# Optimization experiments

Hardware: AMD Instinct MI355X
Metric: run time of the kernel (lower is better)

Reference implementation:

```python
import jax, jax.numpy as jnp
import numpy as np

FREQ_DIM = 64
BLOCK_DIM = 64
N = 256          # lattice sites
CH = 6           # channel_num -> block diagonals at offsets -1, 0, +1
S = 2 * 16 + CH - 2   # seq_num = 36
BS = 4           # block_size (kron of two 2x2 matrices)
HID = 128
EPS = 1e-5
B = 32

_e = np.eye(2)
_sx = np.array([[0., 1.], [1., 0.]])
_siy = np.array([[0., 1.], [-1., 0.]])
_sz = np.array([[1., 0.], [0., -1.]])
_p = [_e, _sx, _siy, _sz]
KRONS = jnp.asarray(np.stack([np.kron(_p[a], _p[b]) for a in range(4) for b in range(4)]).astype(np.float32))  # (16,4,4)
Z1 = KRONS[12]  # kron(sigma_z, I) used for interaction blocks ('z1')


def _bn(h, g, b):
    # BatchNorm1d in training mode: biased batch statistics over axis 0
    mu = h.mean(axis=0)
    v = h.var(axis=0)
    return g * (h - mu) / jnp.sqrt(v + EPS) + b


def _mlp(x, Win, bin_, Wmid, bmid, Wout, bout, gamma, beta):
    # depth-4 MLP: Lin+ReLU, then (BN,Lin,ReLU) x2, then BN,Lin,ReLU
    h = jax.nn.relu(x @ Win + bin_)
    for i in range(Wmid.shape[0]):
        h = jax.nn.relu(_bn(h, gamma[i], beta[i]) @ Wmid[i] + bmid[i])
    return jax.nn.relu(_bn(h, gamma[-1], beta[-1]) @ Wout + bout)


def _lstm(xs, h0, c0, Wih, Whh, bih, bhh):
    # xs: (B, T, S); torch gate order i, f, g, o
    def step(carry, x_t):
        h, c = carry
        gates = x_t @ Wih.T + h @ Whh.T + (bih + bhh)
        i, f, g, o = jnp.split(gates, 4, axis=-1)
        c = jax.nn.sigmoid(f) * c + jax.nn.sigmoid(i) * jnp.tanh(g)
        h = jax.nn.sigmoid(o) * jnp.tanh(c)
        return (h, c), h
    _, hs = jax.lax.scan(step, (h0, c0), jnp.swapaxes(xs, 0, 1))
    return jnp.swapaxes(hs, 0, 1)


def setup_inputs() -> dict:
    key = jax.random.key(0)
    ks = iter(jax.random.split(key, 48))
    def w(shape, s=0.05):
        return jax.random.normal(next(ks), shape, dtype=jnp.float32) * s
    d = {
        'x': w((B, FREQ_DIM + BLOCK_DIM), 1.0),
        'fd_Win': w((FREQ_DIM, HID)), 'fd_bin': w((HID,)),
        'fd_Wmid': w((2, HID, HID)), 'fd_bmid': w((2, HID)),
        'fd_Wout': w((HID, S)), 'fd_bout': w((S,)),
        'fd_gamma': jnp.ones((3, HID), jnp.float32), 'fd_beta': jnp.zeros((3, HID), jnp.float32),
        'bd_Win': w((BLOCK_DIM, HID)), 'bd_bin': w((HID,)),
        'bd_Wmid': w((2, HID, HID)), 'bd_bmid': w((2, HID)),
        'bd_Wout': w((HID, S)), 'bd_bout': w((S,)),
        'bd_gamma': jnp.ones((3, HID), jnp.float32), 'bd_beta': jnp.zeros((3, HID), jnp.float32),
        'sc_Win': w((S, 1, HID)), 'sc_bin': w((S, HID)),
        'sc_Wmid': w((S, 2, HID, HID)), 'sc_bmid': w((S, 2, HID)),
        'sc_Wout': w((S, HID, N)), 'sc_bout': w((S, N)),
        'sc_gamma': jnp.ones((S, 3, HID), jnp.float32), 'sc_beta': jnp.zeros((S, 3, HID), jnp.float32),
        'lstm_Wih': w((4 * S, S)), 'lstm_Whh': w((4 * S, S)),
        'lstm_bih': w((4 * S,)), 'lstm_bhh': w((4 * S,)),
        'mix_W': w((S, 2 * S)), 'mix_b': w((S,)),
    }
    return d


def reference(x, fd_Win, fd_bin, fd_Wmid, fd_bmid, fd_Wout, fd_bout, fd_gamma, fd_beta,
              bd_Win, bd_bin, bd_Wmid, bd_bmid, bd_Wout, bd_bout, bd_gamma, bd_beta,
              sc_Win, sc_bin, sc_Wmid, sc_bmid, sc_Wout, sc_bout, sc_gamma, sc_beta,
              lstm_Wih, lstm_Whh, lstm_bih, lstm_bhh, mix_W, mix_b):
    Bsz = x.shape[0]
    block = _mlp(x[:, FREQ_DIM:], bd_Win, bd_bin, bd_Wmid, bd_bmid, bd_Wout, bd_bout, bd_gamma, bd_beta)  # (B,S)
    freq = _mlp(x[:, :FREQ_DIM], fd_Win, fd_bin, fd_Wmid, fd_bmid, fd_Wout, fd_bout, fd_gamma, fd_beta)   # (B,S)
    # S independent scalar->N MLPs, batched with vmap over the stacked params
    sc = jax.vmap(_mlp)(freq.T[:, :, None], sc_Win, sc_bin, sc_Wmid, sc_bmid,
                        sc_Wout, sc_bout, sc_gamma, sc_beta)  # (S,B,N)
    freq_seq = jnp.cos(sc).transpose(1, 2, 0)   # (B,N,S)
    seq = _lstm(freq_seq, block, jnp.zeros_like(block), lstm_Wih, lstm_Whh, lstm_bih, lstm_bhh)  # (B,N,S)
    block_seq = jnp.concatenate([jnp.broadcast_to(block[:, :, None], (Bsz, S, N)),
                                 jnp.swapaxes(seq, 1, 2)], axis=1)  # (B,2S,N)
    # 1x1 Conv2d == channel mixing matmul
    mixed = jnp.einsum('bcn,oc->bon', block_seq, mix_W) + mix_b[None, :, None]  # (B,S,N)
    inter = mixed[:, :CH - 2]                          # (B,CH-2,N)
    onsite = mixed[:, CH - 2:].reshape(Bsz, 2, 16, N)  # (B,2,16,N)
    H_int = jnp.einsum('bcn,ij->bcnij', inter, Z1)         # (B,CH-2,N,4,4)
    H_os = jnp.einsum('bgkn,kij->bgnij', onsite, KRONS)    # (B,2,N,4,4) summed over 16 pairs
    half = (CH - 2) // 2
    strips = jnp.concatenate([H_int[:, :half], H_os, H_int[:, half:]], axis=1)  # (B,CH,N,4,4)
    strips = strips.reshape(Bsz, CH // 2, 2, N, BS, BS)
    # banded block assembly: strip i lives on block-diagonal offset i - (CH//2)//2
    grid = jnp.zeros((Bsz, 2, N, N, BS, BS), dtype=x.dtype)
    for i in range(CH // 2):
        o = i - (CH // 2) // 2
        rows = jnp.arange(N - abs(o)) + max(0, -o)
        cols = rows + o
        grid = grid.at[:, :, rows, cols].set(strips[:, i][:, :, rows])
    matrix = grid.transpose(0, 1, 2, 4, 3, 5).reshape(Bsz, 2, N * BS, N * BS)
    return matrix
```

## Files before the change

### kernel.cpp

```cpp
#include <hip/hip_runtime.h>
#include <math.h>

#define EPSF 1e-5f
typedef __attribute__((ext_vector_type(2))) float f32x2;
typedef __attribute__((ext_vector_type(4))) float f32x4;

__device__ __forceinline__ float pauliv(int p, int r, int c) {
    switch (p) {
        case 0: return (r == c) ? 1.f : 0.f;
        case 1: return (r != c) ? 1.f : 0.f;
        case 2: return (r == 0 && c == 1) ? 1.f : ((r == 1 && c == 0) ? -1.f : 0.f);
        default: return (r == c) ? ((r == 0) ? 1.f : -1.f) : 0.f;
    }
}

__device__ void mlp64_body(const float* __restrict__ xin,
                           const float* __restrict__ Win,
                           const float* __restrict__ bin_,
                           const float* __restrict__ Wmid,
                           const float* __restrict__ bmid,
                           const float* __restrict__ Wout,
                           const float* __restrict__ bout,
                           const float* __restrict__ gamma,
                           const float* __restrict__ beta,
                           float* __restrict__ out)
{
    __shared__ float sX[2048];
    __shared__ float sA[4096];
    __shared__ float sB[4096];
    __shared__ float sMu[128], sRs[128];
    int tid = threadIdx.x;

    for (int idx = tid; idx < 2048; idx += 512) {
        int b = idx >> 6, c = idx & 63;
        sX[idx] = xin[b * 128 + c];
    }
    __syncthreads();

    for (int idx = tid; idx < 4096; idx += 512) {
        int b = idx >> 7, j = idx & 127;
        float acc = bin_[j];
        for (int c = 0; c < 64; ++c) acc = fmaf(sX[b * 64 + c], Win[c * 128 + j], acc);
        sA[idx] = fmaxf(acc, 0.f);
    }
    __syncthreads();

    float* cur = sA;
    float* nxt = sB;
    for (int l = 0; l < 3; ++l) {
        if (tid < 128) {
            float s = 0.f, s2 = 0.f;
            for (int b = 0; b < 32; ++b) {
                float v = cur[b * 128 + tid];
                s += v; s2 += v * v;
            }
            float mu = s * (1.f / 32.f);
            float var = s2 * (1.f / 32.f) - mu * mu;
            sMu[tid] = mu;
            sRs[tid] = rsqrtf(var + EPSF);
        }
        __syncthreads();
        for (int idx = tid; idx < 4096; idx += 512) {
            int j = idx & 127;
            cur[idx] = gamma[l * 128 + j] * (cur[idx] - sMu[j]) * sRs[j] + beta[l * 128 + j];
        }
        __syncthreads();
        if (l < 2) {
            for (int idx = tid; idx < 4096; idx += 512) {
                int b = idx >> 7, j = idx & 127;
                float acc = bmid[l * 128 + j];
                for (int c = 0; c < 128; ++c)
                    acc = fmaf(cur[b * 128 + c], Wmid[(l * 128 + c) * 128 + j], acc);
                nxt[idx] = fmaxf(acc, 0.f);
            }
            __syncthreads();
            float* t = cur; cur = nxt; nxt = t;
        } else {
            for (int idx = tid; idx < 1152; idx += 512) {
                int b = idx / 36, j = idx - b * 36;
                float acc = bout[j];
                for (int c = 0; c < 128; ++c)
                    acc = fmaf(cur[b * 128 + c], Wout[c * 36 + j], acc);
                out[idx] = fmaxf(acc, 0.f);
            }
        }
    }
}

__global__ __launch_bounds__(512) void k_mlp2(
    const float* __restrict__ x,
    const float* fdWin, const float* fdbin, const float* fdWmid, const float* fdbmid,
    const float* fdWout, const float* fdbout, const float* fdg, const float* fdbt,
    const float* bdWin, const float* bdbin, const float* bdWmid, const float* bdbmid,
    const float* bdWout, const float* bdbout, const float* bdg, const float* bdbt,
    float* freq, float* blk)
{
    if (blockIdx.x == 0)
        mlp64_body(x + 64, bdWin, bdbin, bdWmid, bdbmid, bdWout, bdbout, bdg, bdbt, blk);
    else
        mlp64_body(x, fdWin, fdbin, fdWmid, fdbmid, fdWout, fdbout, fdg, fdbt, freq);
}

__global__ __launch_bounds__(512) void k_sc1(
    const float* __restrict__ freq,
    const float* __restrict__ Win,
    const float* __restrict__ bin_,
    const float* __restrict__ Wmid,
    const float* __restrict__ bmid,
    const float* __restrict__ gamma,
    const float* __restrict__ beta,
    float* __restrict__ actW)
{
    int s = blockIdx.x, tid = threadIdx.x;
    __shared__ float sA[4096];
    __shared__ float sB[4096];
    __shared__ float sMu[128], sRs[128];
    const float* Wm = Wmid + (size_t)s * 2 * 128 * 128;
    const float* gm = gamma + s * 3 * 128;
    const float* bt = beta + s * 3 * 128;

    for (int idx = tid; idx < 4096; idx += 512) {
        int b = idx >> 7, j = idx & 127;
        float acc = fmaf(freq[b * 36 + s], Win[s * 128 + j], bin_[s * 128 + j]);
        sA[idx] = fmaxf(acc, 0.f);
    }
    __syncthreads();

    float* cur = sA;
    float* nxt = sB;
    for (int l = 0; l < 3; ++l) {
        if (tid < 128) {
            float sm = 0.f, s2 = 0.f;
            for (int b = 0; b < 32; ++b) {
                float v = cur[b * 128 + tid];
                sm += v; s2 += v * v;
            }
            float mu = sm * (1.f / 32.f);
            float var = s2 * (1.f / 32.f) - mu * mu;
            sMu[tid] = mu;
            sRs[tid] = rsqrtf(var + EPSF);
        }
        __syncthreads();
        for (int idx = tid; idx < 4096; idx += 512) {
            int j = idx & 127;
            cur[idx] = gm[l * 128 + j] * (cur[idx] - sMu[j]) * sRs[j] + bt[l * 128 + j];
        }
        __syncthreads();
        if (l < 2) {
            int jj = tid & 127, bb = tid >> 7;
            float acc[8];
            #pragma unroll
            for (int k = 0; k < 8; ++k) acc[k] = bmid[(s * 2 + l) * 128 + jj];
            for (int c = 0; c < 128; ++c) {
                float w = Wm[(l * 128 + c) * 128 + jj];
                #pragma unroll
                for (int k = 0; k < 8; ++k)
                    acc[k] = fmaf(cur[(bb + 4 * k) * 128 + c], w, acc[k]);
            }
            __syncthreads();
            #pragma unroll
            for (int k = 0; k < 8; ++k) nxt[(bb + 4 * k) * 128 + jj] = fmaxf(acc[k], 0.f);
            __syncthreads();
            float* t = cur; cur = nxt; nxt = t;
        } else {
            for (int idx = tid; idx < 4096; idx += 512)
                actW[(size_t)s * 4096 + idx] = cur[idx];
        }
    }
}

__global__ __launch_bounds__(512) void k_sc2(
    const float* __restrict__ actW,
    const float* __restrict__ Wout,
    const float* __restrict__ bout,
    float* __restrict__ fseq2)
{
    int bidx = blockIdx.x;
    int s = bidx >> 2, q = bidx & 3;
    int tid = threadIdx.x;
    __shared__ float sAct[4096];
    for (int idx = tid; idx < 4096; idx += 512)
        sAct[idx] = actW[(size_t)s * 4096 + idx];
    __syncthreads();

    int nn = (tid & 63) + q * 64;
    int bb = tid >> 6;
    const float* Wo = Wout + (size_t)s * 128 * 256;
    float acc[4];
    #pragma unroll
    for (int k = 0; k < 4; ++k) acc[k] = bout[s * 256 + nn];
    #pragma unroll 4
    for (int c = 0; c < 128; ++c) {
        float w = Wo[c * 256 + nn];
        #pragma unroll
        for (int k = 0; k < 4; ++k)
            acc[k] = fmaf(sAct[(bb + 8 * k) * 128 + c], w, acc[k]);
    }
    #pragma unroll
    for (int k = 0; k < 4; ++k) {
        float v = fmaxf(acc[k], 0.f);
        fseq2[((size_t)s * 32 + bb + 8 * k) * 256 + nn] = __cosf(v);
    }
}

__global__ __launch_bounds__(512) void k_xg(
    const float* __restrict__ fseq2, const float* __restrict__ Wih,
    const float* __restrict__ bih, const float* __restrict__ bhh,
    float* __restrict__ Xg)
{
    int t = blockIdx.x, tid = threadIdx.x;
    __shared__ float sF[1152];
    __shared__ float sWt[36 * 144];
    for (int idx = tid; idx < 1152; idx += 512) {
        int s = idx >> 5, b = idx & 31;
        sF[b * 36 + s] = fseq2[(size_t)idx * 256 + t];
    }
    for (int idx = tid; idx < 5184; idx += 512) {
        int j = idx / 36, s = idx - j * 36;
        sWt[s * 144 + j] = Wih[idx];
    }
    __syncthreads();
    for (int idx = tid; idx < 4608; idx += 512) {
        int b = idx / 144, j = idx - b * 144;
        int g = j / 36, u = j - g * 36;
        float acc = bih[j] + bhh[j];
        #pragma unroll
        for (int s = 0; s < 36; ++s)
            acc = fmaf(sF[b * 36 + s], sWt[s * 144 + j], acc);
        Xg[(((size_t)b * 256 + t) * 36 + u) * 4 + g] = acc;
    }
}

#define TSTEPS 16
__global__ __launch_bounds__(64, 1) void k_lstm(
    const float* __restrict__ Xg,
    const float* __restrict__ blk,
    const float* __restrict__ Whh,
    float* __restrict__ hseqT)
{
    int b = blockIdx.x;
    int lane = threadIdx.x;
    int uu = lane < 36 ? lane : 35;
    bool active = lane < 36;

    __shared__ float lxg[2][TSTEPS * 144];

    f32x2 wif[36], wgo[36];
    #pragma unroll
    for (int k = 0; k < 36; ++k) {
        wif[k] = f32x2{Whh[uu * 36 + k], Whh[(36 + uu) * 36 + k]};
        wgo[k] = f32x2{Whh[(72 + uu) * 36 + k], Whh[(108 + uu) * 36 + k]};
    }
    float h = blk[b * 36 + uu];
    float c = 0.f;
    const f32x4* xb = (const f32x4*)(Xg + (size_t)b * 256 * 144);
    float* hout = hseqT + ((size_t)b * 36 + uu) * 256;

    f32x4 stg[9];
    #pragma unroll
    for (int i = 0; i < 9; ++i) stg[i] = xb[i * 64 + lane];
    #pragma unroll
    for (int i = 0; i < 9; ++i) ((f32x4*)&lxg[0][0])[i * 64 + lane] = stg[i];

    for (int tt = 0; tt < 256 / TSTEPS; ++tt) {
        const int cur = tt & 1;
        if (tt < 256 / TSTEPS - 1) {
            const f32x4* src = xb + (size_t)(tt + 1) * (TSTEPS * 36);
            #pragma unroll
            for (int i = 0; i < 9; ++i) stg[i] = src[i * 64 + lane];
        }

        #pragma unroll
        for (int s = 0; s < TSTEPS; ++s) {
            f32x4 xg4 = ((const f32x4*)&lxg[cur][s * 144])[uu];
            f32x2 a0 = f32x2{xg4.x, xg4.y};
            f32x2 b0 = f32x2{xg4.z, xg4.w};
            f32x2 a1 = f32x2{0.f, 0.f};
            f32x2 b1 = f32x2{0.f, 0.f};
            #pragma unroll
            for (int k = 0; k < 36; k += 2) {
                float h0 = __int_as_float(__builtin_amdgcn_readlane(__float_as_int(h), k));
                float h1 = __int_as_float(__builtin_amdgcn_readlane(__float_as_int(h), k + 1));
                a0 = __builtin_elementwise_fma(wif[k], f32x2{h0, h0}, a0);
                b0 = __builtin_elementwise_fma(wgo[k], f32x2{h0, h0}, b0);
                a1 = __builtin_elementwise_fma(wif[k + 1], f32x2{h1, h1}, a1);
                b1 = __builtin_elementwise_fma(wgo[k + 1], f32x2{h1, h1}, b1);
            }
            a0 += a1; b0 += b1;
            float iv = 1.f / (1.f + __expf(-a0.x));
            float fv = 1.f / (1.f + __expf(-a0.y));
            float gv = 1.f - 2.f / (__expf(2.f * b0.x) + 1.f);
            float ov = 1.f / (1.f + __expf(-b0.y));
            c = fmaf(fv, c, iv * gv);
            h = ov * (1.f - 2.f / (__expf(2.f * c) + 1.f));
            if (active) hout[tt * TSTEPS + s] = h;
        }

        if (tt < 256 / TSTEPS - 1) {
            #pragma unroll
            for (int i = 0; i < 9; ++i)
                ((f32x4*)&lxg[cur ^ 1][0])[i * 64 + lane] = stg[i];
        }
    }
}

__global__ __launch_bounds__(256) void k_mixed(
    const float* __restrict__ blk, const float* __restrict__ hseqT,
    const float* __restrict__ mixW, const float* __restrict__ mixb,
    float* __restrict__ mixed)
{
    int bq = blockIdx.x;
    int b = bq >> 2, oq = bq & 3;
    int tid = threadIdx.x;
    __shared__ float sH[36 * 256];
    __shared__ float sW[9 * 36];
    __shared__ float sBase[9];
    for (int idx = tid; idx < 9216; idx += 256)
        sH[idx] = hseqT[(size_t)b * 9216 + idx];
    for (int idx = tid; idx < 9 * 36; idx += 256) {
        int o = idx / 36, u = idx - o * 36;
        sW[idx] = mixW[(oq * 9 + o) * 72 + 36 + u];
    }
    if (tid < 9) {
        int o = oq * 9 + tid;
        float acc = mixb[o];
        for (int c = 0; c < 36; ++c) acc = fmaf(mixW[o * 72 + c], blk[b * 36 + c], acc);
        sBase[tid] = acc;
    }
    __syncthreads();
    int n = tid;
    #pragma unroll
    for (int o = 0; o < 9; ++o) {
        float acc = sBase[o];
        #pragma unroll
        for (int u = 0; u < 36; ++u)
            acc = fmaf(sW[o * 36 + u], sH[u * 256 + n], acc);
        mixed[((size_t)b * 36 + oq * 9 + o) * 256 + n] = acc;
    }
}

__global__ __launch_bounds__(256) void k_zero(float* __restrict__ out, long total4)
{
    f32x4* o = (f32x4*)out;
    f32x4 z = f32x4{0.f, 0.f, 0.f, 0.f};
    long stride = (long)gridDim.x * 256;
    for (long i = (long)blockIdx.x * 256 + threadIdx.x; i < total4; i += stride)
        o[i] = z;
}

__global__ __launch_bounds__(256) void k_sparse(
    const float* __restrict__ mixed, float* __restrict__ out)
{
    int bg = blockIdx.x;
    int g = bg & 1, b = bg >> 1;
    int n = threadIdx.x;
    const float* mb = mixed + (size_t)b * 36 * 256;
    float vSub = mb[(size_t)g * 256 + n];
    float vSup = mb[(size_t)(2 + g) * 256 + n];
    float ch[16];
    #pragma unroll
    for (int k = 0; k < 16; ++k) ch[k] = mb[(size_t)(4 + 16 * g + k) * 256 + n];
    float d[16];
    #pragma unroll
    for (int e = 0; e < 16; ++e) {
        int r = e >> 2, cc = e & 3;
        float acc = 0.f;
        #pragma unroll
        for (int k = 0; k < 16; ++k) {
            float kv = pauliv(k >> 2, r >> 1, cc >> 1) * pauliv(k & 3, r & 1, cc & 1);
            if (kv == 1.f) acc = acc + ch[k];
            else if (kv == -1.f) acc = acc - ch[k];
        }
        d[e] = acc;
    }

    float* base = out + (size_t)bg * 1024 * 1024;
    #pragma unroll
    for (int r = 0; r < 4; ++r)
        *(f32x4*)(base + (size_t)(4 * n + r) * 1024 + 4 * n) =
            f32x4{d[r * 4 + 0], d[r * 4 + 1], d[r * 4 + 2], d[r * 4 + 3]};
    if (n > 0) {
        #pragma unroll
        for (int r = 0; r < 4; ++r)
            base[(size_t)(4 * n + r) * 1024 + 4 * (n - 1) + r] = (r < 2) ? vSub : -vSub;
    }
    if (n < 255) {
        #pragma unroll
        for (int r = 0; r < 4; ++r)
            base[(size_t)(4 * n + r) * 1024 + 4 * (n + 1) + r] = (r < 2) ? vSup : -vSup;
    }
}

extern "C" void kernel_launch(void* const* d_in, const int* in_sizes, int n_in,
                              void* d_out, int out_size, void* d_ws, size_t ws_size,
                              hipStream_t stream) {
    const float* x      = (const float*)d_in[0];
    const float* fdWin  = (const float*)d_in[1];
    const float* fdbin  = (const float*)d_in[2];
    const float* fdWmid = (const float*)d_in[3];
    const float* fdbmid = (const float*)d_in[4];
    const float* fdWout = (const float*)d_in[5];
    const float* fdbout = (const float*)d_in[6];
    const float* fdg    = (const float*)d_in[7];
    const float* fdbt   = (const float*)d_in[8];
    const float* bdWin  = (const float*)d_in[9];
    const float* bdbin  = (const float*)d_in[10];
    const float* bdWmid = (const float*)d_in[11];
    const float* bdbmid = (const float*)d_in[12];
    const float* bdWout = (const float*)d_in[13];
    const float* bdbout = (const float*)d_in[14];
    const float* bdg    = (const float*)d_in[15];
    const float* bdbt   = (const float*)d_in[16];
    const float* scWin  = (const float*)d_in[17];
    const float* scbin  = (const float*)d_in[18];
    const float* scWmid = (const float*)d_in[19];
    const float* scbmid = (const float*)d_in[20];
    const float* scWout = (const float*)d_in[21];
    const float* scbout = (const float*)d_in[22];
    const float* scg    = (const float*)d_in[23];
    const float* scbt   = (const float*)d_in[24];
    const float* Wih    = (const float*)d_in[25];
    const float* Whh    = (const float*)d_in[26];
    const float* bih    = (const float*)d_in[27];
    const float* bhh    = (const float*)d_in[28];
    const float* mixW   = (const float*)d_in[29];
    const float* mixb   = (const float*)d_in[30];

    float* ws    = (float*)d_ws;
    float* freq  = ws;
    float* blk   = ws + 1152;
    float* fseq2 = ws + 2304;
    float* Xg    = ws + 297216;
    float* hseqT = ws + 1476864;
    float* mixed = ws + 1771776;
    float* actW  = Xg;

    float* out = (float*)d_out;
    long total4 = (long)out_size / 4;

    k_zero<<<2048, 256, 0, stream>>>(out, total4);
    k_mlp2<<<2, 512, 0, stream>>>(x,
        fdWin, fdbin, fdWmid, fdbmid, fdWout, fdbout, fdg, fdbt,
        bdWin, bdbin, bdWmid, bdbmid, bdWout, bdbout, bdg, bdbt,
        freq, blk);
    k_sc1<<<36, 512, 0, stream>>>(freq, scWin, scbin, scWmid, scbmid, scg, scbt, actW);
    k_sc2<<<144, 512, 0, stream>>>(actW, scWout, scbout, fseq2);
    k_xg<<<256, 512, 0, stream>>>(fseq2, Wih, bih, bhh, Xg);
    k_lstm<<<32, 64, 0, stream>>>(Xg, blk, Whh, hseqT);
    k_mixed<<<128, 256, 0, stream>>>(blk, hseqT, mixW, mixb, mixed);
    k_sparse<<<64, 256, 0, stream>>>(mixed, out);
}
```

Measured before the change: 315.1 us.

## Fuse output zeroing with band scatter, register-prefetch LSTM inputs, widen MLP block

The separate zero-fill and sparse-scatter kernels are merged into one kernel. Each block zeroes a 32-row chunk of the output and then writes the banded blocks for the 8 sites in that chunk, which removes one launch and a pass over the output. The LSTM drops its shared-memory double buffer in favour of an 8-deep register prefetch ring and writes h in time-major order, so k_mixed now reads through a padded shared tile. The MLP kernel moves to 1024 threads per block. The tradeoffs are more write-ordering dependence inside each block and a possible occupancy or register-pressure change in the LSTM.

Result: slower. 350.9 us (+11.4%).

```diff
diff --git a/kernel.cpp b/kernel.cpp
--- a/kernel.cpp
+++ b/kernel.cpp
@@ -31,13 +31,13 @@
     __shared__ float sMu[128], sRs[128];
     int tid = threadIdx.x;
 
-    for (int idx = tid; idx < 2048; idx += 512) {
+    for (int idx = tid; idx < 2048; idx += 1024) {
         int b = idx >> 6, c = idx & 63;
         sX[idx] = xin[b * 128 + c];
     }
     __syncthreads();
 
-    for (int idx = tid; idx < 4096; idx += 512) {
+    for (int idx = tid; idx < 4096; idx += 1024) {
         int b = idx >> 7, j = idx & 127;
         float acc = bin_[j];
         for (int c = 0; c < 64; ++c) acc = fmaf(sX[b * 64 + c], Win[c * 128 + j], acc);
@@ -60,13 +60,13 @@
             sRs[tid] = rsqrtf(var + EPSF);
         }
         __syncthreads();
-        for (int idx = tid; idx < 4096; idx += 512) {
+        for (int idx = tid; idx < 4096; idx += 1024) {
             int j = idx & 127;
             cur[idx] = gamma[l * 128 + j] * (cur[idx] - sMu[j]) * sRs[j] + beta[l * 128 + j];
         }
         __syncthreads();
         if (l < 2) {
-            for (int idx = tid; idx < 4096; idx += 512) {
+            for (int idx = tid; idx < 4096; idx += 1024) {
                 int b = idx >> 7, j = idx & 127;
                 float acc = bmid[l * 128 + j];
                 for (int c = 0; c < 128; ++c)
@@ -76,7 +76,7 @@
             __syncthreads();
             float* t = cur; cur = nxt; nxt = t;
         } else {
-            for (int idx = tid; idx < 1152; idx += 512) {
+            for (int idx = tid; idx < 1152; idx += 1024) {
                 int b = idx / 36, j = idx - b * 36;
                 float acc = bout[j];
                 for (int c = 0; c < 128; ++c)
@@ -87,7 +87,7 @@
     }
 }
 
-__global__ __launch_bounds__(512) void k_mlp2(
+__global__ __launch_bounds__(1024) void k_mlp2(
     const float* __restrict__ x,
     const float* fdWin, const float* fdbin, const float* fdWmid, const float* fdbmid,
     const float* fdWout, const float* fdbout, const float* fdg, const float* fdbt,
@@ -231,20 +231,18 @@
     }
 }
 
-#define TSTEPS 16
+#define PF 8
 __global__ __launch_bounds__(64, 1) void k_lstm(
     const float* __restrict__ Xg,
     const float* __restrict__ blk,
     const float* __restrict__ Whh,
-    float* __restrict__ hseqT)
+    float* __restrict__ hseq2)
 {
     int b = blockIdx.x;
     int lane = threadIdx.x;
     int uu = lane < 36 ? lane : 35;
     bool active = lane < 36;
 
-    __shared__ float lxg[2][TSTEPS * 144];
-
     f32x2 wif[36], wgo[36];
     #pragma unroll
     for (int k = 0; k < 36; ++k) {
@@ -254,69 +252,56 @@
     float h = blk[b * 36 + uu];
     float c = 0.f;
     const f32x4* xb = (const f32x4*)(Xg + (size_t)b * 256 * 144);
-    float* hout = hseqT + ((size_t)b * 36 + uu) * 256;
-
-    f32x4 stg[9];
-    #pragma unroll
-    for (int i = 0; i < 9; ++i) stg[i] = xb[i * 64 + lane];
-    #pragma unroll
-    for (int i = 0; i < 9; ++i) ((f32x4*)&lxg[0][0])[i * 64 + lane] = stg[i];
-
-    for (int tt = 0; tt < 256 / TSTEPS; ++tt) {
-        const int cur = tt & 1;
-        if (tt < 256 / TSTEPS - 1) {
-            const f32x4* src = xb + (size_t)(tt + 1) * (TSTEPS * 36);
-            #pragma unroll
-            for (int i = 0; i < 9; ++i) stg[i] = src[i * 64 + lane];
-        }
-
-        #pragma unroll
-        for (int s = 0; s < TSTEPS; ++s) {
-            f32x4 xg4 = ((const f32x4*)&lxg[cur][s * 144])[uu];
-            f32x2 a0 = f32x2{xg4.x, xg4.y};
-            f32x2 b0 = f32x2{xg4.z, xg4.w};
-            f32x2 a1 = f32x2{0.f, 0.f};
-            f32x2 b1 = f32x2{0.f, 0.f};
-            #pragma unroll
-            for (int k = 0; k < 36; k += 2) {
-                float h0 = __int_as_float(__builtin_amdgcn_readlane(__float_as_int(h), k));
-                float h1 = __int_as_float(__builtin_amdgcn_readlane(__float_as_int(h), k + 1));
-                a0 = __builtin_elementwise_fma(wif[k], f32x2{h0, h0}, a0);
-                b0 = __builtin_elementwise_fma(wgo[k], f32x2{h0, h0}, b0);
-                a1 = __builtin_elementwise_fma(wif[k + 1], f32x2{h1, h1}, a1);
-                b1 = __builtin_elementwise_fma(wgo[k + 1], f32x2{h1, h1}, b1);
-            }
-            a0 += a1; b0 += b1;
-            float iv = 1.f / (1.f + __expf(-a0.x));
-            float fv = 1.f / (1.f + __expf(-a0.y));
-            float gv = 1.f - 2.f / (__expf(2.f * b0.x) + 1.f);
-            float ov = 1.f / (1.f + __expf(-b0.y));
-            c = fmaf(fv, c, iv * gv);
-            h = ov * (1.f - 2.f / (__expf(2.f * c) + 1.f));
-            if (active) hout[tt * TSTEPS + s] = h;
-        }
-
-        if (tt < 256 / TSTEPS - 1) {
-            #pragma unroll
-            for (int i = 0; i < 9; ++i)
-                ((f32x4*)&lxg[cur ^ 1][0])[i * 64 + lane] = stg[i];
-        }
+    float* hout = hseq2 + (size_t)b * 256 * 36;
+
+    f32x4 pipe[PF];
+    #pragma unroll
+    for (int i = 0; i < PF; ++i) pipe[i] = xb[i * 36 + uu];
+
+    #pragma unroll 8
+    for (int t = 0; t < 256; ++t) {
+        f32x4 xg4 = pipe[t & (PF - 1)];
+        if (t + PF < 256) pipe[t & (PF - 1)] = xb[(t + PF) * 36 + uu];
+
+        f32x2 a0 = f32x2{xg4.x, xg4.y};
+        f32x2 b0 = f32x2{xg4.z, xg4.w};
+        f32x2 a1 = f32x2{0.f, 0.f};
+        f32x2 b1 = f32x2{0.f, 0.f};
+        #pragma unroll
+        for (int k = 0; k < 36; k += 2) {
+            float h0 = __int_as_float(__builtin_amdgcn_readlane(__float_as_int(h), k));
+            float h1 = __int_as_float(__builtin_amdgcn_readlane(__float_as_int(h), k + 1));
+            a0 = __builtin_elementwise_fma(wif[k], f32x2{h0, h0}, a0);
+            b0 = __builtin_elementwise_fma(wgo[k], f32x2{h0, h0}, b0);
+            a1 = __builtin_elementwise_fma(wif[k + 1], f32x2{h1, h1}, a1);
+            b1 = __builtin_elementwise_fma(wgo[k + 1], f32x2{h1, h1}, b1);
+        }
+        a0 += a1; b0 += b1;
+        float iv = 1.f / (1.f + __expf(-a0.x));
+        float fv = 1.f / (1.f + __expf(-a0.y));
+        float gv = 1.f - 2.f / (__expf(2.f * b0.x) + 1.f);
+        float ov = 1.f / (1.f + __expf(-b0.y));
+        c = fmaf(fv, c, iv * gv);
+        h = ov * (1.f - 2.f / (__expf(2.f * c) + 1.f));
+        if (active) hout[t * 36 + uu] = h;
     }
 }
 
 __global__ __launch_bounds__(256) void k_mixed(
-    const float* __restrict__ blk, const float* __restrict__ hseqT,
+    const float* __restrict__ blk, const float* __restrict__ hseq2,
     const float* __restrict__ mixW, const float* __restrict__ mixb,
     float* __restrict__ mixed)
 {
     int bq = blockIdx.x;
     int b = bq >> 2, oq = bq & 3;
     int tid = threadIdx.x;
-    __shared__ float sH[36 * 256];
+    __shared__ float sH[256 * 37];
     __shared__ float sW[9 * 36];
     __shared__ float sBase[9];
-    for (int idx = tid; idx < 9216; idx += 256)
-        sH[idx] = hseqT[(size_t)b * 9216 + idx];
+    for (int idx = tid; idx < 9216; idx += 256) {
+        int t = idx / 36, u = idx - t * 36;
+        sH[t * 37 + u] = hseq2[(size_t)b * 9216 + idx];
+    }
     for (int idx = tid; idx < 9 * 36; idx += 256) {
         int o = idx / 36, u = idx - o * 36;
         sW[idx] = mixW[(oq * 9 + o) * 72 + 36 + u];
@@ -334,60 +319,61 @@
         float acc = sBase[o];
         #pragma unroll
         for (int u = 0; u < 36; ++u)
-            acc = fmaf(sW[o * 36 + u], sH[u * 256 + n], acc);
+            acc = fmaf(sW[o * 36 + u], sH[n * 37 + u], acc);
         mixed[((size_t)b * 36 + oq * 9 + o) * 256 + n] = acc;
     }
 }
 
-__global__ __launch_bounds__(256) void k_zero(float* __restrict__ out, long total4)
-{
-    f32x4* o = (f32x4*)out;
+__global__ __launch_bounds__(256) void k_out(
+    const float* __restrict__ mixed, float* __restrict__ out)
+{
+    int bid = blockIdx.x;
+    int bg = bid >> 5, chunk = bid & 31;
+    int g = bg & 1, b = bg >> 1;
+    float* base = out + (size_t)bg * (1024 * 1024);
+    f32x4* rp = (f32x4*)(base + (size_t)chunk * 32 * 1024);
     f32x4 z = f32x4{0.f, 0.f, 0.f, 0.f};
-    long stride = (long)gridDim.x * 256;
-    for (long i = (long)blockIdx.x * 256 + threadIdx.x; i < total4; i += stride)
-        o[i] = z;
-}
-
-__global__ __launch_bounds__(256) void k_sparse(
-    const float* __restrict__ mixed, float* __restrict__ out)
-{
-    int bg = blockIdx.x;
-    int g = bg & 1, b = bg >> 1;
-    int n = threadIdx.x;
-    const float* mb = mixed + (size_t)b * 36 * 256;
-    float vSub = mb[(size_t)g * 256 + n];
-    float vSup = mb[(size_t)(2 + g) * 256 + n];
-    float ch[16];
-    #pragma unroll
-    for (int k = 0; k < 16; ++k) ch[k] = mb[(size_t)(4 + 16 * g + k) * 256 + n];
-    float d[16];
-    #pragma unroll
-    for (int e = 0; e < 16; ++e) {
-        int r = e >> 2, cc = e & 3;
-        float acc = 0.f;
-        #pragma unroll
-        for (int k = 0; k < 16; ++k) {
-            float kv = pauliv(k >> 2, r >> 1, cc >> 1) * pauliv(k & 3, r & 1, cc & 1);
-            if (kv == 1.f) acc = acc + ch[k];
-            else if (kv == -1.f) acc = acc - ch[k];
-        }
-        d[e] = acc;
-    }
-
-    float* base = out + (size_t)bg * 1024 * 1024;
-    #pragma unroll
-    for (int r = 0; r < 4; ++r)
-        *(f32x4*)(base + (size_t)(4 * n + r) * 1024 + 4 * n) =
-            f32x4{d[r * 4 + 0], d[r * 4 + 1], d[r * 4 + 2], d[r * 4 + 3]};
-    if (n > 0) {
+    #pragma unroll
+    for (int i = 0; i < 32; ++i)
+        rp[i * 256 + threadIdx.x] = z;
+    __syncthreads();
+
+    int tid = threadIdx.x;
+    if (tid < 8) {
+        int n = chunk * 8 + tid;
+        const float* mb = mixed + (size_t)b * 36 * 256;
+        float vSub = mb[(size_t)g * 256 + n];
+        float vSup = mb[(size_t)(2 + g) * 256 + n];
+        float ch[16];
+        #pragma unroll
+        for (int k = 0; k < 16; ++k) ch[k] = mb[(size_t)(4 + 16 * g + k) * 256 + n];
+        float d[16];
+        #pragma unroll
+        for (int e = 0; e < 16; ++e) {
+            int r = e >> 2, cc = e & 3;
+            float acc = 0.f;
+            #pragma unroll
+            for (int k = 0; k < 16; ++k) {
+                float kv = pauliv(k >> 2, r >> 1, cc >> 1) * pauliv(k & 3, r & 1, cc & 1);
+                if (kv == 1.f) acc = acc + ch[k];
+                else if (kv == -1.f) acc = acc - ch[k];
+            }
+            d[e] = acc;
+        }
         #pragma unroll
         for (int r = 0; r < 4; ++r)
-            base[(size_t)(4 * n + r) * 1024 + 4 * (n - 1) + r] = (r < 2) ? vSub : -vSub;
-    }
-    if (n < 255) {
-        #pragma unroll
-        for (int r = 0; r < 4; ++r)
-            base[(size_t)(4 * n + r) * 1024 + 4 * (n + 1) + r] = (r < 2) ? vSup : -vSup;
+            *(f32x4*)(base + (size_t)(4 * n + r) * 1024 + 4 * n) =
+                f32x4{d[r * 4 + 0], d[r * 4 + 1], d[r * 4 + 2], d[r * 4 + 3]};
+        if (n > 0) {
+            #pragma unroll
+            for (int r = 0; r < 4; ++r)
+                base[(size_t)(4 * n + r) * 1024 + 4 * (n - 1) + r] = (r < 2) ? vSub : -vSub;
+        }
+        if (n < 255) {
+            #pragma unroll
+            for (int r = 0; r < 4; ++r)
+                base[(size_t)(4 * n + r) * 1024 + 4 * (n + 1) + r] = (r < 2) ? vSup : -vSup;
+        }
     }
 }
 
@@ -431,22 +417,20 @@
     float* blk   = ws + 1152;
     float* fseq2 = ws + 2304;
     float* Xg    = ws + 297216;
-    float* hseqT = ws + 1476864;
+    float* hseq2 = ws + 1476864;
     float* mixed = ws + 1771776;
     float* actW  = Xg;
 
     float* out = (float*)d_out;
-    long total4 = (long)out_size / 4;
-
-    k_zero<<<2048, 256, 0, stream>>>(out, total4);
-    k_mlp2<<<2, 512, 0, stream>>>(x,
+
+    k_mlp2<<<2, 1024, 0, stream>>>(x,
         fdWin, fdbin, fdWmid, fdbmid, fdWout, fdbout, fdg, fdbt,
         bdWin, bdbin, bdWmid, bdbmid, bdWout, bdbout, bdg, bdbt,
         freq, blk);
     k_sc1<<<36, 512, 0, stream>>>(freq, scWin, scbin, scWmid, scbmid, scg, scbt, actW);
     k_sc2<<<144, 512, 0, stream>>>(actW, scWout, scbout, fseq2);
     k_xg<<<256, 512, 0, stream>>>(fseq2, Wih, bih, bhh, Xg);
-    k_lstm<<<32, 64, 0, stream>>>(Xg, blk, Whh, hseqT);
-    k_mixed<<<128, 256, 0, stream>>>(blk, hseqT, mixW, mixb, mixed);
-    k_sparse<<<64, 256, 0, stream>>>(mixed, out);
-}
+    k_lstm<<<32, 64, 0, stream>>>(Xg, blk, Whh, hseq2);
+    k_mixed<<<128, 256, 0, stream>>>(blk, hseq2, mixW, mixb, mixed);
+    k_out<<<2048, 256, 0, stream>>>(mixed, out);
+}
```
